# Kernel optimization log

Hardware: AMD Instinct MI355X
Metric: run time of the kernel (lower is better)

Reference implementation:

```python
import jax, jax.numpy as jnp
import numpy as np

B_GRAPHS = 16
N_PER_GRAPH = 128
N_NODES = B_GRAPHS * N_PER_GRAPH  # 2048
HIDDEN = 256
N_HEADS = 8
HEAD_DIM = HIDDEN // N_HEADS
N_LAYERS = 4
K_RPE = 4
N_EDGES = 32768
NUM_NODE_FEATS = 32
NUM_EDGE_TYPES = 16
MAX_DEGREE = 100
MLP_HID = HIDDEN // 2


def _layernorm(x, s, b):
    m = x.mean(-1, keepdims=True)
    v = jnp.var(x, axis=-1, keepdims=True)
    return (x - m) / jnp.sqrt(v + 1e-5) * s + b


def setup_inputs() -> dict:
    key = jax.random.key(0)
    ks = jax.random.split(key, 24)
    s = 0.02
    x_idx = jax.random.randint(ks[0], (N_NODES,), 0, NUM_NODE_FEATS)
    # edges are intra-graph (the torch code drops cross-graph edges)
    src = jax.random.randint(ks[1], (N_EDGES,), 0, N_NODES)
    dst = (src // N_PER_GRAPH) * N_PER_GRAPH + jax.random.randint(ks[2], (N_EDGES,), 0, N_PER_GRAPH)
    edge_index = jnp.stack([src, dst])
    edge_attr = jax.random.randint(ks[3], (N_EDGES,), 0, NUM_EDGE_TYPES)
    batch = jnp.repeat(jnp.arange(B_GRAPHS), N_PER_GRAPH)
    L = N_LAYERS
    return {
        'x_idx': x_idx, 'edge_index': edge_index, 'edge_attr': edge_attr, 'batch': batch,
        'node_emb': jax.random.normal(ks[4], (NUM_NODE_FEATS, HIDDEN)) * s,
        'edge_emb': jax.random.normal(ks[5], (NUM_EDGE_TYPES, N_HEADS)) * s,
        'degree_emb': jax.random.normal(ks[6], (MAX_DEGREE + 1, HIDDEN)) * s,
        'rpe_W1': jax.random.normal(ks[7], (K_RPE + 1, MLP_HID)) * s,
        'rpe_b1': jnp.zeros((MLP_HID,)),
        'rpe_W2': jax.random.normal(ks[8], (MLP_HID, N_HEADS)) * s,
        'rpe_b2': jnp.zeros((N_HEADS,)),
        'Wq': jax.random.normal(ks[9], (L, HIDDEN, HIDDEN)) * s, 'bq': jnp.zeros((L, HIDDEN)),
        'Wk': jax.random.normal(ks[10], (L, HIDDEN, HIDDEN)) * s, 'bk': jnp.zeros((L, HIDDEN)),
        'Wv': jax.random.normal(ks[11], (L, HIDDEN, HIDDEN)) * s, 'bv': jnp.zeros((L, HIDDEN)),
        'Wo': jax.random.normal(ks[12], (L, HIDDEN, HIDDEN)) * s, 'bo': jnp.zeros((L, HIDDEN)),
        'ln1_s': jnp.ones((L, HIDDEN)), 'ln1_b': jnp.zeros((L, HIDDEN)),
        'ln2_s': jnp.ones((L, HIDDEN)), 'ln2_b': jnp.zeros((L, HIDDEN)),
        'ff_W1': jax.random.normal(ks[13], (L, HIDDEN, 2 * HIDDEN)) * s, 'ff_b1': jnp.zeros((L, 2 * HIDDEN)),
        'ff_W2': jax.random.normal(ks[14], (L, 2 * HIDDEN, HIDDEN)) * s, 'ff_b2': jnp.zeros((L, HIDDEN)),
    }


def _forward(x_idx, edge_index, edge_attr, batch,
             node_emb, edge_emb, degree_emb, rpe_W1, rpe_b1, rpe_W2, rpe_b2,
             Wq, bq, Wk, bk, Wv, bv, Wo, bo, ln1_s, ln1_b, ln2_s, ln2_b,
             ff_W1, ff_b1, ff_W2, ff_b2):
    B, n, H, N = B_GRAPHS, N_PER_GRAPH, N_HEADS, N_NODES
    x = node_emb[x_idx]                               # [N, d]
    src, dst = edge_index[0], edge_index[1]
    # degrees from source endpoints (scatter_add in torch)
    deg = jnp.zeros((N,), jnp.int32).at[src].add(1)
    deg_c = jnp.minimum(deg, MAX_DEGREE)

    # ---- RRWP + edge-type attention bias, block-diagonal over graphs ----
    g = batch[src]
    intra = (batch[src] == batch[dst])                # torch code skips cross-graph edges
    u = src % n
    v = dst % n
    intra_f = intra.astype(jnp.float32)
    inv_du = intra_f / jnp.maximum(deg[src], 1).astype(jnp.float32)
    inv_dv = intra_f / jnp.maximum(deg[dst], 1).astype(jnp.float32)
    # random-walk transition matrix per graph [B, n, n]
    T = (jnp.zeros((B, n, n), jnp.float32)
         .at[g, u, v].add(inv_du)
         .at[g, v, u].add(inv_dv))
    # symmetric edge-type bias per graph [B, n, n, H]
    ev = edge_emb[edge_attr] * intra_f[:, None]
    EB = (jnp.zeros((B, n, n, H), jnp.float32)
          .at[g, u, v].add(ev)
          .at[g, v, u].add(ev))
    # walk powers I, T, T^2, ..., T^K -> [B, n, n, K+1]
    I = jnp.broadcast_to(jnp.eye(n, dtype=jnp.float32), (B, n, n))
    powers = [I, T]
    cur = T
    for _ in range(2, K_RPE + 1):
        cur = cur @ T
        powers.append(cur)
    walk = jnp.stack(powers, axis=-1)
    pair = jax.nn.relu(walk @ rpe_W1 + rpe_b1) @ rpe_W2 + rpe_b2   # [B, n, n, H]
    block = (pair + EB).transpose(0, 3, 1, 2)                      # [B, H, n, n]
    ib = jnp.arange(B)
    full = jnp.full((H, B, n, B, n), -jnp.inf, jnp.float32)
    full = full.at[:, ib, :, ib, :].set(block)                     # diag blocks
    attn_bias = full.reshape(H, N, N)

    # ---- transformer stack ----
    deg_vec = degree_emb[deg_c]
    scale = 1.0 / jnp.sqrt(jnp.float32(HEAD_DIM))
    for l in range(N_LAYERS):
        x = x + deg_vec
        Q = (x @ Wq[l] + bq[l]).reshape(N, H, HEAD_DIM)
        K_ = (x @ Wk[l] + bk[l]).reshape(N, H, HEAD_DIM)
        V = (x @ Wv[l] + bv[l]).reshape(N, H, HEAD_DIM)
        scores = jnp.einsum('ihd,jhd->hij', Q, K_) * scale + attn_bias
        aw = jax.nn.softmax(scores, axis=-1)
        out = jnp.einsum('hij,jhd->ihd', aw, V).reshape(N, HIDDEN)
        out = out @ Wo[l] + bo[l]
        x = _layernorm(x + out, ln1_s[l], ln1_b[l])
        ff = jax.nn.relu(x @ ff_W1[l] + ff_b1[l]) @ ff_W2[l] + ff_b2[l]
        x = _layernorm(x + ff, ln2_s[l], ln2_b[l])
    # global add pool
    return jax.ops.segment_sum(x, batch, num_segments=B)


def reference(x_idx, edge_index, edge_attr, batch,
              node_emb, edge_emb, degree_emb, rpe_W1, rpe_b1, rpe_W2, rpe_b2,
              Wq, bq, Wk, bk, Wv, bv, Wo, bo, ln1_s, ln1_b, ln2_s, ln2_b,
              ff_W1, ff_b1, ff_W2, ff_b2):
    return _forward(x_idx, edge_index, edge_attr, batch,
                    node_emb, edge_emb, degree_emb, rpe_W1, rpe_b1, rpe_W2, rpe_b2,
                    Wq, bq, Wk, bk, Wv, bv, Wo, bo, ln1_s, ln1_b, ln2_s, ln2_b,
                    ff_W1, ff_b1, ff_W2, ff_b2)
```

## Files before the change

kernel.cpp:

```cpp
#include <hip/hip_runtime.h>
#include <hip/hip_bf16.h>

#define B_GRAPHS 16
#define NPG 128
#define NN 2048
#define HIDDEN 256
#define N_HEADS 8
#define HEAD_DIM 32
#define N_LAYERS 4
#define N_EDGES 32768
#define MLP_HID 128
#define MAX_DEG 100

typedef __hip_bfloat16 bf16;
typedef unsigned short ushort_t;
typedef __attribute__((ext_vector_type(8))) short short8;
typedef __attribute__((ext_vector_type(4))) float f32x4;

__device__ __forceinline__ float us2f(ushort_t u) {
    return __uint_as_float(((unsigned)u) << 16);
}
__device__ __forceinline__ ushort_t f2us(float f) {
    unsigned u = __float_as_uint(f);
    return (ushort_t)((u + 0x7FFFu + ((u >> 16) & 1u)) >> 16);
}
__device__ __forceinline__ bool is_bf16_mode(const unsigned* probe) {
    return probe[0] != 0x3F800000u;
}
#define MFMA16(a, b, c) __builtin_amdgcn_mfma_f32_16x16x32_bf16(a, b, c, 0, 0, 0)

__device__ __forceinline__ void gload_lds16(const void* g, void* l) {
    __builtin_amdgcn_global_load_lds(
        (const __attribute__((address_space(1))) unsigned int*)g,
        (__attribute__((address_space(3))) unsigned int*)l, 16, 0, 0);
}
#define SBAR __builtin_amdgcn_s_barrier()
#define WAITP8 asm volatile("s_waitcnt vmcnt(8) lgkmcnt(0)" ::: "memory")
#define WAITLAST asm volatile("s_waitcnt vmcnt(0) lgkmcnt(0)" ::: "memory")
#define LBAR do { asm volatile("s_waitcnt lgkmcnt(0)" ::: "memory"); SBAR; \
                  asm volatile("" ::: "memory"); } while (0)

#define NW 23
__device__ const int c_wsizes[NW] = {
    8192, 128, 25856, 640, 128, 1024, 8,
    262144, 1024, 262144, 1024, 262144, 1024, 262144, 1024,
    1024, 1024, 1024, 1024,
    524288, 2048, 524288, 1024};
#define TOTW 2144392

#define OFF_NODE_EMB 0
#define OFF_EDGE_EMB 8192
#define OFF_DEG_EMB  8320
#define OFF_RPE_W1   34176
#define OFF_RPE_B1   34816
#define OFF_RPE_W2   34944
#define OFF_RPE_B2   35968
#define OFF_BO       1087624
#define OFF_LN1S     1088648
#define OFF_LN1B     1089672
#define OFF_LN2S     1090696
#define OFF_LN2B     1091720
#define OFF_FFB1     1617032
#define OFF_FFB2     2143368

#define WB_QKV 0
#define WB_O   786432
#define WB_F1  1048576
#define WB_F2  1572864
#define WB_TOT 2097152
#define QKVB_TOT 3072

#define ZERO_BLKS 2310
#define CONV_BLKS 8389
#define TP_BLKS   2048

struct SrcPtrs { const void* p[NW]; };

__global__ __launch_bounds__(256) void prep1(SrcPtrs sp, const unsigned* __restrict__ probe,
                                             float* __restrict__ Wc, float* __restrict__ qkvb,
                                             f32x4* __restrict__ zerop,
                                             ushort_t* __restrict__ WB) {
    __shared__ float tile[32][33];
    int b = blockIdx.x;
    bool isbf = is_bf16_mode(probe);
    auto rd = [&](int seg, int off) -> float {
        return isbf ? us2f(((const ushort_t*)sp.p[seg])[off])
                    : ((const float*)sp.p[seg])[off];
    };
    if (b < ZERO_BLKS) {
        f32x4 z;
        z[0] = 0.f; z[1] = 0.f; z[2] = 0.f; z[3] = 0.f;
        zerop[b * 256 + threadIdx.x] = z;
    } else if (b < ZERO_BLKS + CONV_BLKS) {
        int i = (b - ZERO_BLKS) * 256 + threadIdx.x;
        if (i < TOTW) {
            int seg = 0, off = i;
            while (seg < NW - 1 && off >= c_wsizes[seg]) { off -= c_wsizes[seg]; seg++; }
            bool dead = (seg == 7 || seg == 9 || seg == 11 || seg == 13 ||
                         seg == 19 || seg == 21);
            if (!dead) Wc[i] = rd(seg, off);
        } else if (i < TOTW + QKVB_TOT) {
            int j = i - TOTW;
            int l = j / 768, n = j % 768, which = n >> 8, nn = n & 255;
            int seg = (which == 0) ? 8 : (which == 1) ? 10 : 12;
            qkvb[j] = rd(seg, l * 256 + nn);
        }
    } else {
        int tb = b - ZERO_BLKS - CONV_BLKS;
        int seg, soff, srcN, k0, n0, dK;
        size_t doff;
        if (tb < 768) {
            int mat = tb >> 6, t = tb & 63;
            int l = mat / 3, which = mat % 3;
            seg = 7 + which * 2;
            soff = l * 65536; srcN = 256;
            k0 = (t >> 3) * 32; n0 = (t & 7) * 32;
            doff = (size_t)l * 196608 + (size_t)which * 65536; dK = 256;
        } else if (tb < 1024) {
            int u = tb - 768, l = u >> 6, t = u & 63;
            seg = 13; soff = l * 65536; srcN = 256;
            k0 = (t >> 3) * 32; n0 = (t & 7) * 32;
            doff = WB_O + (size_t)l * 65536; dK = 256;
        } else if (tb < 1536) {
            int u = tb - 1024, l = u >> 7, t = u & 127;
            seg = 19; soff = l * 131072; srcN = 512;
            k0 = (t >> 4) * 32; n0 = (t & 15) * 32;
            doff = WB_F1 + (size_t)l * 131072; dK = 256;
        } else {
            int u = tb - 1536, l = u >> 7, t = u & 127;
            seg = 21; soff = l * 131072; srcN = 256;
            k0 = (t >> 3) * 32; n0 = (t & 7) * 32;
            doff = WB_F2 + (size_t)l * 131072; dK = 512;
        }
        int xcol = threadIdx.x & 31, y8 = threadIdx.x >> 5;
        const void* srcp = sp.p[seg];
#pragma unroll
        for (int rr = 0; rr < 4; rr++) {
            int row = y8 * 4 + rr;
            int off = soff + (k0 + row) * srcN + n0 + xcol;
            tile[row][xcol] = isbf ? us2f(((const ushort_t*)srcp)[off])
                                   : ((const float*)srcp)[off];
        }
        __syncthreads();
#pragma unroll
        for (int rr = 0; rr < 4; rr++) {
            int nrow = y8 * 4 + rr;
            WB[doff + (size_t)(n0 + nrow) * dK + k0 + xcol] = f2us(tile[xcol][nrow]);
        }
    }
}

__global__ void deg_kernel(const int* __restrict__ src, int* __restrict__ deg) {
    int e = blockIdx.x * blockDim.x + threadIdx.x;
    if (e < N_EDGES) atomicAdd(&deg[src[e]], 1);
}

__global__ void prep2(const int* __restrict__ xidx, const int* __restrict__ deg,
                      const float* __restrict__ emb, const float* __restrict__ demb,
                      float* __restrict__ x, ushort_t* __restrict__ xb,
                      const int* __restrict__ ei, const int* __restrict__ eattr,
                      const int* __restrict__ batch, const float* __restrict__ edge_emb,
                      float* __restrict__ T, float* __restrict__ bias) {
    int b = blockIdx.x;
    if (b < 2048) {
        int i = b * 256 + threadIdx.x;
        int node = i >> 8, c = i & 255;
        float v = emb[xidx[node] * HIDDEN + c] + demb[min(deg[node], MAX_DEG) * HIDDEN + c];
        x[i] = v;
        xb[i] = f2us(v);
    } else {
        int idx = (b - 2048) * 256 + threadIdx.x;
        int e = idx >> 3, h = idx & 7;
        int s = ei[e], d = ei[N_EDGES + e];
        if (batch[s] != batch[d]) return;
        int g = batch[s];
        int u = s & (NPG - 1), v = d & (NPG - 1);
        if (h == 0) {
            atomicAdd(&T[(g * NPG + u) * NPG + v], 1.0f / (float)max(deg[s], 1));
            atomicAdd(&T[(g * NPG + v) * NPG + u], 1.0f / (float)max(deg[d], 1));
        }
        float ev = edge_emb[eattr[e] * N_HEADS + h];
        atomicAdd(&bias[(((size_t)(g * N_HEADS + h) * NPG + u) * NPG + v)], ev);
        atomicAdd(&bias[(((size_t)(g * N_HEADS + h) * NPG + v) * NPG + u)], ev);
    }
}

__global__ __launch_bounds__(256) void matmul128(const float* __restrict__ A,
                                                 const float* __restrict__ B,
                                                 float* __restrict__ C) {
    int g = blockIdx.x >> 4, t8 = blockIdx.x & 15;
    int col = threadIdx.x & 127, half = threadIdx.x >> 7;
    const float* Ag = A + (size_t)g * NPG * NPG;
    const float* Bg = B + (size_t)g * NPG * NPG;
    __shared__ float arow[8][NPG];
    for (int i = threadIdx.x; i < 8 * NPG; i += 256)
        arow[i >> 7][i & 127] = Ag[(t8 * 8 + (i >> 7)) * NPG + (i & 127)];
    __syncthreads();
    float acc[4] = {0.f, 0.f, 0.f, 0.f};
#pragma unroll 8
    for (int k = 0; k < NPG; k++) {
        float bv = Bg[k * NPG + col];
#pragma unroll
        for (int r = 0; r < 4; r++) acc[r] += arow[half * 4 + r][k] * bv;
    }
#pragma unroll
    for (int r = 0; r < 4; r++)
        C[((size_t)g * NPG + t8 * 8 + half * 4 + r) * NPG + col] = acc[r];
}

__global__ __launch_bounds__(256) void matmul128_dual(const float* __restrict__ T2,
                                                      const float* __restrict__ T,
                                                      float* __restrict__ T3,
                                                      float* __restrict__ T4) {
    int which = blockIdx.x >> 8;
    int bid = blockIdx.x & 255;
    int g = bid >> 4, t8 = bid & 15;
    int col = threadIdx.x & 127, half = threadIdx.x >> 7;
    const float* Ag = T2 + (size_t)g * NPG * NPG;
    const float* Bg = (which ? T2 : T) + (size_t)g * NPG * NPG;
    float* Cg = (which ? T4 : T3) + (size_t)g * NPG * NPG;
    __shared__ float arow[8][NPG];
    for (int i = threadIdx.x; i < 8 * NPG; i += 256)
        arow[i >> 7][i & 127] = Ag[(t8 * 8 + (i >> 7)) * NPG + (i & 127)];
    __syncthreads();
    float acc[4] = {0.f, 0.f, 0.f, 0.f};
#pragma unroll 8
    for (int k = 0; k < NPG; k++) {
        float bv = Bg[k * NPG + col];
#pragma unroll
        for (int r = 0; r < 4; r++) acc[r] += arow[half * 4 + r][k] * bv;
    }
#pragma unroll
    for (int r = 0; r < 4; r++)
        Cg[(t8 * 8 + half * 4 + r) * NPG + col] = acc[r];
}

__global__ __launch_bounds__(256) void rpe_kernel(
    const float* __restrict__ T, const float* __restrict__ T2,
    const float* __restrict__ T3, const float* __restrict__ T4,
    const float* __restrict__ W1, const float* __restrict__ b1,
    const float* __restrict__ W2, const float* __restrict__ b2,
    float* __restrict__ bias) {
    int g = blockIdx.x >> 7, i = blockIdx.x & 127;
    int w = threadIdx.x >> 6, lane = threadIdx.x & 63;
    int lr = lane & 15, lq = lane >> 4;
    __shared__ __align__(16) ushort_t hid[4][4096];

    int pbase = (g * 128 + i) * 128;
    int j0w = w * 32;

    f32x4 zero;
    zero[0] = 0.f; zero[1] = 0.f; zero[2] = 0.f; zero[3] = 0.f;

    short8 b1f[8];
#pragma unroll
    for (int nt = 0; nt < 8; nt++) {
        short8 v{};
        if (lq == 0) {
            int n = nt * 16 + lr;
#pragma unroll
            for (int e = 0; e < 5; e++) v[e] = (short)f2us(W1[e * 128 + n]);
        }
        b1f[nt] = v;
    }
    short8 b2f[4];
#pragma unroll
    for (int kt = 0; kt < 4; kt++) {
        short8 v{};
        if (lr < 8) {
#pragma unroll
            for (int e = 0; e < 8; e++)
                v[e] = (short)f2us(W2[(kt * 32 + lq * 8 + e) * 8 + lr]);
        }
        b2f[kt] = v;
    }
    float b1v[8];
#pragma unroll
    for (int nt = 0; nt < 8; nt++) b1v[nt] = b1[nt * 16 + lr];
    float b2v = (lr < 8) ? b2[lr] : 0.f;

#pragma unroll
    for (int mt = 0; mt < 2; mt++) {
        int j0 = j0w + mt * 16;
        short8 af{};
        if (lq == 0) {
            int p = pbase + j0 + lr;
            af[0] = (short)f2us((i == j0 + lr) ? 1.f : 0.f);
            af[1] = (short)f2us(T[p]);
            af[2] = (short)f2us(T2[p]);
            af[3] = (short)f2us(T3[p]);
            af[4] = (short)f2us(T4[p]);
        }
        f32x4 h[8];
#pragma unroll
        for (int nt = 0; nt < 8; nt++) h[nt] = MFMA16(af, b1f[nt], zero);
#pragma unroll
        for (int nt = 0; nt < 8; nt++) {
#pragma unroll
            for (int r = 0; r < 4; r++) {
                int row = mt * 16 + lq * 4 + r;
                int colb = (nt * 32 + lr * 2) ^ ((row & 7) << 4);
                *(ushort_t*)((char*)&hid[w][0] + row * 256 + colb) =
                    f2us(fmaxf(h[nt][r] + b1v[nt], 0.f));
            }
        }
    }
    asm volatile("s_waitcnt lgkmcnt(0)" ::: "memory");

#pragma unroll
    for (int mt = 0; mt < 2; mt++) {
        f32x4 o;
        o[0] = 0.f; o[1] = 0.f; o[2] = 0.f; o[3] = 0.f;
#pragma unroll
        for (int kt = 0; kt < 4; kt++) {
            int row = mt * 16 + lr;
            int colb = (kt * 64 + lq * 16) ^ ((lr & 7) << 4);
            short8 a = *(const short8*)((const char*)&hid[w][0] + row * 256 + colb);
            o = MFMA16(a, b2f[kt], o);
        }
        if (lr < 8) {
            size_t base2 = (((size_t)(g * N_HEADS + lr) * NPG + i) * NPG) + j0w + mt * 16;
#pragma unroll
            for (int r = 0; r < 4; r++)
                bias[base2 + lq * 4 + r] += o[r] + b2v;
        }
    }
}

__global__ __launch_bounds__(512, 1) void qkv_attn(
    const ushort_t* __restrict__ x_bf, const ushort_t* __restrict__ WT,
    const float* __restrict__ qb, const float* __restrict__ bias,
    ushort_t* __restrict__ ao) {
    int g = blockIdx.x >> 3, h = blockIdx.x & 7;
    int o = threadIdx.x >> 6, lane = threadIdx.x & 63;
    int lr = lane & 15, lq = lane >> 4;

    __shared__ char Wbuf[3][16384];
    __shared__ ushort_t Ks[NPG][40];
    __shared__ ushort_t VT[32][136];
    __shared__ ushort_t P[8][16][136];

    const ushort_t* xg = x_bf + (size_t)g * NPG * HIDDEN;
    int row16 = o * 16;

    short8 Ax[8];
#pragma unroll
    for (int kk = 0; kk < 8; kk++)
        Ax[kk] = *(const short8*)(xg + (size_t)(row16 + lr) * 256 + kk * 32 + lq * 8);
    float bqv[2], bkv[2], bvv[2];
#pragma unroll
    for (int j = 0; j < 2; j++) {
        int c = h * 32 + j * 16 + lr;
        bqv[j] = qb[c]; bkv[j] = qb[256 + c]; bvv[j] = qb[512 + c];
    }
    __builtin_amdgcn_sched_barrier(0);

    auto stageW = [&](int rowbase, int c) {
        const char* gW = (const char*)WT;
        char* lb = &Wbuf[c][0] + o * 2048;
#pragma unroll
        for (int it = 0; it < 2; it++) {
            int j = o * 2048 + it * 1024 + lane * 16;
            int n = j >> 9, off = j & 511;
            gload_lds16(gW + (size_t)(rowbase + n) * 512 + (off ^ ((n & 7) << 4)),
                        lb + it * 1024);
        }
        __builtin_amdgcn_sched_barrier(0);
    };
    stageW(h * 32, 0);
    stageW(256 + h * 32, 1);
    stageW(512 + h * 32, 2);

    auto rdW = [&](int c, int jt, int kk) -> short8 {
        int n = jt * 16 + lr;
        int off = n * 512 + ((kk * 64 + lq * 16) ^ ((n & 7) << 4));
        return *(const short8*)(&Wbuf[c][off]);
    };

    f32x4 qa[2]{}, ka[2]{}, va[2]{};
    asm volatile("s_waitcnt vmcnt(4)" ::: "memory"); SBAR;
#pragma unroll
    for (int kk = 0; kk < 8; kk++)
#pragma unroll
        for (int j = 0; j < 2; j++)
            qa[j] = MFMA16(Ax[kk], rdW(0, j, kk), qa[j]);

    const float* bg = bias + (size_t)(g * N_HEADS + h) * NPG * NPG;
    float bgv[8][4];
#pragma unroll
    for (int r = 0; r < 4; r++) {
        int i = row16 + lq * 4 + r;
#pragma unroll
        for (int jt = 0; jt < 8; jt++)
            bgv[jt][r] = bg[(size_t)i * NPG + jt * 16 + lr];
    }
    __builtin_amdgcn_sched_barrier(0);

    asm volatile("s_waitcnt vmcnt(34)" ::: "memory"); SBAR;
#pragma unroll
    for (int kk = 0; kk < 8; kk++)
#pragma unroll
        for (int j = 0; j < 2; j++)
            ka[j] = MFMA16(Ax[kk], rdW(1, j, kk), ka[j]);

    asm volatile("s_waitcnt vmcnt(32)" ::: "memory"); SBAR;
#pragma unroll
    for (int kk = 0; kk < 8; kk++)
#pragma unroll
        for (int j = 0; j < 2; j++)
            va[j] = MFMA16(Ax[kk], rdW(2, j, kk), va[j]);

#pragma unroll
    for (int j = 0; j < 2; j++) {
        int c = j * 16 + lr;
#pragma unroll
        for (int r = 0; r < 4; r++) {
            int row = row16 + lq * 4 + r;
            P[o][lq * 4 + r][c] = f2us(qa[j][r] + bqv[j]);
            Ks[row][c] = f2us(ka[j][r] + bkv[j]);
            VT[c][row] = f2us(va[j][r] + bvv[j]);
        }
    }
    __syncthreads();

    short8 qf = *(const short8*)(&P[o][lr][lq * 8]);
    f32x4 S[8];
    f32x4 zero;
    zero[0] = 0.f; zero[1] = 0.f; zero[2] = 0.f; zero[3] = 0.f;
#pragma unroll
    for (int jt = 0; jt < 8; jt++) {
        short8 kf = *(const short8*)(&Ks[jt * 16 + lr][lq * 8]);
        S[jt] = MFMA16(qf, kf, zero);
    }

    const float scale = 0.17677669529663687f;
    float lrow[4];
#pragma unroll
    for (int r = 0; r < 4; r++) {
        float mx = -1e30f;
#pragma unroll
        for (int jt = 0; jt < 8; jt++) {
            float s = S[jt][r] * scale + bgv[jt][r];
            S[jt][r] = s;
            mx = fmaxf(mx, s);
        }
#pragma unroll
        for (int m = 1; m < 16; m <<= 1) mx = fmaxf(mx, __shfl_xor(mx, m));
        float sum = 0.f;
#pragma unroll
        for (int jt = 0; jt < 8; jt++) {
            float e = __expf(S[jt][r] - mx);
            S[jt][r] = e;
            sum += e;
        }
#pragma unroll
        for (int m = 1; m < 16; m <<= 1) sum += __shfl_xor(sum, m);
        lrow[r] = sum;
    }

#pragma unroll
    for (int jt = 0; jt < 8; jt++)
#pragma unroll
        for (int r = 0; r < 4; r++)
            P[o][lq * 4 + r][jt * 16 + lr] = f2us(S[jt][r]);

    f32x4 O[2]{};
#pragma unroll
    for (int k0 = 0; k0 < NPG; k0 += 32) {
        short8 pa = *(const short8*)(&P[o][lr][k0 + lq * 8]);
#pragma unroll
        for (int dt = 0; dt < 2; dt++) {
            short8 vb = *(const short8*)(&VT[dt * 16 + lr][k0 + lq * 8]);
            O[dt] = MFMA16(pa, vb, O[dt]);
        }
    }
#pragma unroll
    for (int r = 0; r < 4; r++) {
        float inv = 1.f / lrow[r];
        int row = g * NPG + row16 + lq * 4 + r;
#pragma unroll
        for (int dt = 0; dt < 2; dt++)
            ao[(size_t)row * HIDDEN + h * 32 + dt * 16 + lr] = f2us(O[dt][r] * inv);
    }
}

__global__ __launch_bounds__(512, 2) void fused_mlp(
    const ushort_t* __restrict__ ao, const ushort_t* __restrict__ WoT,
    const float* __restrict__ bo, const float* __restrict__ ln1s,
    const float* __restrict__ ln1b,
    const ushort_t* __restrict__ F1T, const ushort_t* __restrict__ F2T,
    const float* __restrict__ fb1, const float* __restrict__ fb2,
    const float* __restrict__ ln2s, const float* __restrict__ ln2b,
    const float* __restrict__ xin, const int* __restrict__ deg,
    const float* __restrict__ demb, int add_deg,
    float* __restrict__ xout, ushort_t* __restrict__ xb,
    float* __restrict__ poolf, int do_pool) {
    int m0 = blockIdx.x * 8;
    int wave = threadIdx.x >> 6, lane = threadIdx.x & 63;
    int lr = lane & 15, lq = lane >> 4;
    int ar = m0 + (lr & 7);

    __shared__ ushort_t Wbuf[2][32768];
    __shared__ ushort_t xs_bf[8][264];
    __shared__ ushort_t ffh[8][520];
    __shared__ float ws[8][16], qs[8][16];

    auto stageO = [&](int h, int b) {
        const char* gW = (const char*)WoT;
        char* lb = (char*)&Wbuf[b][0] + wave * 8192;
#pragma unroll
        for (int it = 0; it < 8; it++) {
            int j = wave * 8192 + it * 1024 + lane * 16;
            int n = j >> 8, off = j & 255;
            gload_lds16(gW + n * 512 + h * 256 + (off ^ ((n & 7) << 4)), lb + it * 1024);
        }
        __builtin_amdgcn_sched_barrier(0);
    };
    auto stageF1 = [&](int q, int b) {
        const char* gW = (const char*)F1T;
        char* lb = (char*)&Wbuf[b][0] + wave * 8192;
#pragma unroll
        for (int it = 0; it < 8; it++) {
            int j = wave * 8192 + it * 1024 + lane * 16;
            int n = j >> 9, off = j & 511;
            gload_lds16(gW + (q * 128 + n) * 512 + (off ^ ((n & 7) << 4)), lb + it * 1024);
        }
        __builtin_amdgcn_sched_barrier(0);
    };
    auto stageF2 = [&](int q, int b) {
        const char* gW = (const char*)F2T;
        char* lb = (char*)&Wbuf[b][0] + wave * 8192;
#pragma unroll
        for (int it = 0; it < 8; it++) {
            int j = wave * 8192 + it * 1024 + lane * 16;
            int n = j >> 8, off = j & 255;
            gload_lds16(gW + n * 1024 + q * 256 + (off ^ ((n & 7) << 4)), lb + it * 1024);
        }
        __builtin_amdgcn_sched_barrier(0);
    };

    float bo_v[2], l1s[2], l1b[2], fb2v[2], l2s[2], l2b[2], xres[2][4], fb1q[4];
#pragma unroll
    for (int jt = 0; jt < 2; jt++) {
        int col = wave * 32 + jt * 16 + lr;
        bo_v[jt] = bo[col]; l1s[jt] = ln1s[col]; l1b[jt] = ln1b[col];
        fb2v[jt] = fb2[col]; l2s[jt] = ln2s[col]; l2b[jt] = ln2b[col];
#pragma unroll
        for (int r = 0; r < 4; r++) {
            int row = m0 + ((lq * 4 + r) & 7);
            xres[jt][r] = xin[(size_t)row * 256 + col];
        }
    }
#pragma unroll
    for (int q = 0; q < 4; q++) fb1q[q] = fb1[q * 128 + wave * 16 + lr];
    int dg4[4];
    if (add_deg) {
#pragma unroll
        for (int r = 0; r < 4; r++)
            dg4[r] = min(deg[m0 + ((lq * 4 + r) & 7)], MAX_DEG);
    }
    short8 Af[8];
#pragma unroll
    for (int t = 0; t < 8; t++)
        Af[t] = *(const short8*)(ao + (size_t)ar * 256 + t * 32 + lq * 8);

    stageO(0, 0);
    stageO(1, 1);

    f32x4 acc[2]{};
#pragma unroll
    for (int h = 0; h < 2; h++) {
        WAITP8; SBAR; asm volatile("" ::: "memory");
#pragma unroll
        for (int kk = 0; kk < 4; kk++) {
            short8 a = Af[h * 4 + kk];
#pragma unroll
            for (int jt = 0; jt < 2; jt++) {
                int n = wave * 32 + jt * 16 + lr;
                int bo_ = n * 256 + ((kk * 64 + lq * 16) ^ ((n & 7) << 4));
                short8 bf = *(const short8*)((const char*)&Wbuf[h][0] + bo_);
                acc[jt] = MFMA16(a, bf, acc[jt]);
            }
        }
        LBAR;
        if (h == 0) stageF1(0, 0);
        else        stageF1(1, 1);
    }

    float valLN[2][4];
#pragma unroll
    for (int r = 0; r < 4; r++) {
        float s = 0.f, s2 = 0.f;
#pragma unroll
        for (int jt = 0; jt < 2; jt++) {
            float v = acc[jt][r] + bo_v[jt] + xres[jt][r];
            valLN[jt][r] = v;
            s += v;
            s2 += v * v;
        }
#pragma unroll
        for (int m = 1; m < 16; m <<= 1) {
            s += __shfl_xor(s, m);
            s2 += __shfl_xor(s2, m);
        }
        if (lr == 0) { ws[wave][lq * 4 + r] = s; qs[wave][lq * 4 + r] = s2; }
    }
    LBAR;
#pragma unroll
    for (int r = 0; r < 4; r++) {
        int rr = lq * 4 + r;
        float sum = 0.f, sum2 = 0.f;
#pragma unroll
        for (int c = 0; c < 8; c++) { sum += ws[c][rr]; sum2 += qs[c][rr]; }
        float mean = sum * (1.f / 256.f);
        float var = sum2 * (1.f / 256.f) - mean * mean;
        float rstd = rsqrtf(var + 1e-5f);
#pragma unroll
        for (int jt = 0; jt < 2; jt++) {
            int col = wave * 32 + jt * 16 + lr;
            float y = (valLN[jt][r] - mean) * rstd * l1s[jt] + l1b[jt];
            valLN[jt][r] = y;
            if (rr < 8) xs_bf[rr][col] = f2us(y);
        }
    }

#pragma unroll
    for (int q = 0; q < 4; q++) {
        WAITP8; SBAR; asm volatile("" ::: "memory");
        f32x4 a1{};
        int nl = wave * 16 + lr;
#pragma unroll
        for (int kk = 0; kk < 8; kk++) {
            short8 a = *(const short8*)(&xs_bf[lr & 7][kk * 32 + lq * 8]);
            int bo_ = nl * 512 + ((kk * 64 + lq * 16) ^ ((nl & 7) << 4));
            short8 bf = *(const short8*)((const char*)&Wbuf[q & 1][0] + bo_);
            a1 = MFMA16(a, bf, a1);
        }
        int col = q * 128 + wave * 16 + lr;
#pragma unroll
        for (int r = 0; r < 4; r++) {
            int rr = lq * 4 + r;
            if (rr < 8) ffh[rr][col] = f2us(fmaxf(a1[r] + fb1q[q], 0.f));
        }
        LBAR;
        if (q < 2) stageF1(q + 2, q & 1);
        else       stageF2(q - 2, q & 1);
    }

    f32x4 acc2[2]{};
#pragma unroll
    for (int q = 0; q < 4; q++) {
        if (q == 3) { WAITLAST; } else { WAITP8; }
        SBAR; asm volatile("" ::: "memory");
#pragma unroll
        for (int kk = 0; kk < 4; kk++) {
            short8 a = *(const short8*)(&ffh[lr & 7][q * 128 + kk * 32 + lq * 8]);
#pragma unroll
            for (int jt = 0; jt < 2; jt++) {
                int n = wave * 32 + jt * 16 + lr;
                int bo_ = n * 256 + ((kk * 64 + lq * 16) ^ ((n & 7) << 4));
                short8 bf = *(const short8*)((const char*)&Wbuf[q & 1][0] + bo_);
                acc2[jt] = MFMA16(a, bf, acc2[jt]);
            }
        }
        LBAR;
        if (q < 2) stageF2(q + 2, q & 1);
    }

    float val2[2][4];
#pragma unroll
    for (int r = 0; r < 4; r++) {
        int rr = lq * 4 + r;
        float s = 0.f, s2 = 0.f;
#pragma unroll
        for (int jt = 0; jt < 2; jt++) {
            float v = acc2[jt][r] + fb2v[jt] + valLN[jt][r];
            val2[jt][r] = v;
            s += v;
            s2 += v * v;
        }
#pragma unroll
        for (int m = 1; m < 16; m <<= 1) {
            s += __shfl_xor(s, m);
            s2 += __shfl_xor(s2, m);
        }
        if (lr == 0) { ws[wave][rr] = s; qs[wave][rr] = s2; }
    }
    __syncthreads();
    float psum[2] = {0.f, 0.f};
#pragma unroll
    for (int r = 0; r < 4; r++) {
        int rr = lq * 4 + r;
        float sum = 0.f, sum2 = 0.f;
#pragma unroll
        for (int c = 0; c < 8; c++) { sum += ws[c][rr]; sum2 += qs[c][rr]; }
        float mean = sum * (1.f / 256.f);
        float var = sum2 * (1.f / 256.f) - mean * mean;
        float rstd = rsqrtf(var + 1e-5f);
        if (rr < 8) {
            int row = m0 + rr;
#pragma unroll
            for (int jt = 0; jt < 2; jt++) {
                int col = wave * 32 + jt * 16 + lr;
                float y = (val2[jt][r] - mean) * rstd * l2s[jt] + l2b[jt];
                if (add_deg) y += demb[dg4[r] * 256 + col];
                xout[(size_t)row * 256 + col] = y;
                xb[(size_t)row * 256 + col] = f2us(y);
                if (do_pool) psum[jt] += y;
            }
        }
    }
    if (do_pool && lq < 2) {
        int g = m0 >> 7;
#pragma unroll
        for (int jt = 0; jt < 2; jt++) {
            int col = wave * 32 + jt * 16 + lr;
            atomicAdd(&poolf[g * 256 + col], psum[jt]);
        }
    }
}

__global__ void pool_kernel(const float* __restrict__ poolf, void* __restrict__ out,
                            const unsigned* __restrict__ probe) {
    int i = blockIdx.x * 256 + threadIdx.x;
    float acc = poolf[i];
    if (is_bf16_mode(probe))
        ((bf16*)out)[i] = __float2bfloat16(acc);
    else
        ((float*)out)[i] = acc;
}

extern "C" void kernel_launch(void* const* d_in, const int* in_sizes, int n_in,
                              void* d_out, int out_size, void* d_ws, size_t ws_size,
                              hipStream_t stream) {
    const int* x_idx      = (const int*)d_in[0];
    const int* edge_index = (const int*)d_in[1];
    const int* edge_attr  = (const int*)d_in[2];
    const int* batch      = (const int*)d_in[3];
    const unsigned* probe = (const unsigned*)d_in[19];

    char* base = (char*)d_ws;
    float* Wc    = (float*)base;       base += (size_t)TOTW * 4;
    float* x     = (float*)base;       base += (size_t)NN * HIDDEN * 4;
    float* T     = (float*)base;       base += 262144 * 4;
    float* bias  = (float*)base;       base += (size_t)2097152 * 4;
    int*   deg   = (int*)base;         base += 2048 * 4;
    float* poolf = (float*)base;       base += 4096 * 4;
    float* T2    = (float*)base;       base += 262144 * 4;
    float* T3    = (float*)base;       base += 262144 * 4;
    float* T4    = (float*)base;       base += 262144 * 4;
    float* qkvb  = (float*)base;       base += QKVB_TOT * 4;
    ushort_t* WB    = (ushort_t*)base; base += (size_t)WB_TOT * 2;
    ushort_t* x_bf  = (ushort_t*)base; base += (size_t)NN * HIDDEN * 2;
    ushort_t* ao_bf = (ushort_t*)base; base += (size_t)NN * HIDDEN * 2;

    SrcPtrs sp;
    for (int i = 0; i < NW; i++) sp.p[i] = d_in[4 + i];

    prep1<<<ZERO_BLKS + CONV_BLKS + TP_BLKS, 256, 0, stream>>>(sp, probe, Wc, qkvb,
                                                               (f32x4*)T, WB);
    deg_kernel<<<N_EDGES / 256, 256, 0, stream>>>(edge_index, deg);
    prep2<<<3072, 256, 0, stream>>>(x_idx, deg, Wc + OFF_NODE_EMB, Wc + OFF_DEG_EMB,
                                    x, x_bf, edge_index, edge_attr, batch,
                                    Wc + OFF_EDGE_EMB, T, bias);
    matmul128<<<256, 256, 0, stream>>>(T, T, T2);
    matmul128_dual<<<512, 256, 0, stream>>>(T2, T, T3, T4);
    rpe_kernel<<<B_GRAPHS * NPG, 256, 0, stream>>>(
        T, T2, T3, T4, Wc + OFF_RPE_W1, Wc + OFF_RPE_B1, Wc + OFF_RPE_W2, Wc + OFF_RPE_B2,
        bias);

    for (int l = 0; l < N_LAYERS; l++) {
        qkv_attn<<<B_GRAPHS * N_HEADS, 512, 0, stream>>>(
            x_bf, WB + WB_QKV + (size_t)l * 196608, qkvb + l * 768, bias, ao_bf);
        fused_mlp<<<NN / 8, 512, 0, stream>>>(
            ao_bf, WB + WB_O + (size_t)l * 65536, Wc + OFF_BO + l * 256,
            Wc + OFF_LN1S + l * 256, Wc + OFF_LN1B + l * 256,
            WB + WB_F1 + (size_t)l * 131072, WB + WB_F2 + (size_t)l * 131072,
            Wc + OFF_FFB1 + l * 512, Wc + OFF_FFB2 + l * 256,
            Wc + OFF_LN2S + l * 256, Wc + OFF_LN2B + l * 256, x,
            deg, Wc + OFF_DEG_EMB, (l < N_LAYERS - 1) ? 1 : 0, x, x_bf,
            poolf, (l == N_LAYERS - 1) ? 1 : 0);
    }
    pool_kernel<<<16, 256, 0, stream>>>(poolf, d_out, probe);
}
```

Measured before the change: 308.2 us.

## Fuse T3/T4 matmuls into RPE MLP kernel via shared-memory rows

Merges the dual 128x128 matmul kernel that computed T3=T2@T and T4=T2@T2 into the RPE MLP kernel. Each block computes 8 rows of T3/T4 into shared memory and runs the MFMA MLP on them directly, so the T3/T4 global buffers and one launch go away. The grid shrinks from 2048 blocks to 256, and each wave now handles 8x more (i,j) pairs serially, which may reduce parallelism and latency hiding.

```diff
diff --git a/kernel.cpp b/kernel.cpp
--- a/kernel.cpp
+++ b/kernel.cpp
@@ -208,46 +208,22 @@
         C[((size_t)g * NPG + t8 * 8 + half * 4 + r) * NPG + col] = acc[r];
 }
 
-__global__ __launch_bounds__(256) void matmul128_dual(const float* __restrict__ T2,
-                                                      const float* __restrict__ T,
-                                                      float* __restrict__ T3,
-                                                      float* __restrict__ T4) {
-    int which = blockIdx.x >> 8;
-    int bid = blockIdx.x & 255;
-    int g = bid >> 4, t8 = bid & 15;
-    int col = threadIdx.x & 127, half = threadIdx.x >> 7;
-    const float* Ag = T2 + (size_t)g * NPG * NPG;
-    const float* Bg = (which ? T2 : T) + (size_t)g * NPG * NPG;
-    float* Cg = (which ? T4 : T3) + (size_t)g * NPG * NPG;
-    __shared__ float arow[8][NPG];
-    for (int i = threadIdx.x; i < 8 * NPG; i += 256)
-        arow[i >> 7][i & 127] = Ag[(t8 * 8 + (i >> 7)) * NPG + (i & 127)];
-    __syncthreads();
-    float acc[4] = {0.f, 0.f, 0.f, 0.f};
-#pragma unroll 8
-    for (int k = 0; k < NPG; k++) {
-        float bv = Bg[k * NPG + col];
-#pragma unroll
-        for (int r = 0; r < 4; r++) acc[r] += arow[half * 4 + r][k] * bv;
-    }
-#pragma unroll
-    for (int r = 0; r < 4; r++)
-        Cg[(t8 * 8 + half * 4 + r) * NPG + col] = acc[r];
-}
-
-__global__ __launch_bounds__(256) void rpe_kernel(
-    const float* __restrict__ T, const float* __restrict__ T2,
-    const float* __restrict__ T3, const float* __restrict__ T4,
+__global__ __launch_bounds__(256) void dual_rpe(
+    const float* __restrict__ T, const float* __restrict__ T2c,
     const float* __restrict__ W1, const float* __restrict__ b1,
     const float* __restrict__ W2, const float* __restrict__ b2,
     float* __restrict__ bias) {
-    int g = blockIdx.x >> 7, i = blockIdx.x & 127;
-    int w = threadIdx.x >> 6, lane = threadIdx.x & 63;
+    int g = blockIdx.x >> 4, t8 = blockIdx.x & 15;
+    int tid = threadIdx.x;
+    int w = tid >> 6, lane = tid & 63;
     int lr = lane & 15, lq = lane >> 4;
+
+    __shared__ float arow[8][NPG];
+    __shared__ float T3L[8][NPG], T4L[8][NPG];
     __shared__ __align__(16) ushort_t hid[4][4096];
 
-    int pbase = (g * 128 + i) * 128;
-    int j0w = w * 32;
+    const float* Tg  = T   + (size_t)g * NPG * NPG;
+    const float* T2g = T2c + (size_t)g * NPG * NPG;
 
     f32x4 zero;
     zero[0] = 0.f; zero[1] = 0.f; zero[2] = 0.f; zero[3] = 0.f;
@@ -279,50 +255,83 @@
     for (int nt = 0; nt < 8; nt++) b1v[nt] = b1[nt * 16 + lr];
     float b2v = (lr < 8) ? b2[lr] : 0.f;
 
-#pragma unroll
-    for (int mt = 0; mt < 2; mt++) {
-        int j0 = j0w + mt * 16;
-        short8 af{};
-        if (lq == 0) {
-            int p = pbase + j0 + lr;
-            af[0] = (short)f2us((i == j0 + lr) ? 1.f : 0.f);
-            af[1] = (short)f2us(T[p]);
-            af[2] = (short)f2us(T2[p]);
-            af[3] = (short)f2us(T3[p]);
-            af[4] = (short)f2us(T4[p]);
-        }
-        f32x4 h[8];
-#pragma unroll
-        for (int nt = 0; nt < 8; nt++) h[nt] = MFMA16(af, b1f[nt], zero);
-#pragma unroll
-        for (int nt = 0; nt < 8; nt++) {
+    int col = tid & 127, half = tid >> 7;
+    for (int i = tid; i < 8 * NPG; i += 256)
+        arow[i >> 7][i & 127] = T2g[(t8 * 8 + (i >> 7)) * NPG + (i & 127)];
+    __syncthreads();
+    {
+        float a3[4] = {0.f, 0.f, 0.f, 0.f}, a4[4] = {0.f, 0.f, 0.f, 0.f};
+#pragma unroll 8
+        for (int k = 0; k < NPG; k++) {
+            float bv3 = Tg[k * NPG + col];
+            float bv4 = T2g[k * NPG + col];
 #pragma unroll
             for (int r = 0; r < 4; r++) {
-                int row = mt * 16 + lq * 4 + r;
-                int colb = (nt * 32 + lr * 2) ^ ((row & 7) << 4);
-                *(ushort_t*)((char*)&hid[w][0] + row * 256 + colb) =
-                    f2us(fmaxf(h[nt][r] + b1v[nt], 0.f));
+                float av = arow[half * 4 + r][k];
+                a3[r] += av * bv3;
+                a4[r] += av * bv4;
             }
         }
-    }
-    asm volatile("s_waitcnt lgkmcnt(0)" ::: "memory");
-
-#pragma unroll
-    for (int mt = 0; mt < 2; mt++) {
-        f32x4 o;
-        o[0] = 0.f; o[1] = 0.f; o[2] = 0.f; o[3] = 0.f;
-#pragma unroll
-        for (int kt = 0; kt < 4; kt++) {
-            int row = mt * 16 + lr;
-            int colb = (kt * 64 + lq * 16) ^ ((lr & 7) << 4);
-            short8 a = *(const short8*)((const char*)&hid[w][0] + row * 256 + colb);
-            o = MFMA16(a, b2f[kt], o);
-        }
-        if (lr < 8) {
-            size_t base2 = (((size_t)(g * N_HEADS + lr) * NPG + i) * NPG) + j0w + mt * 16;
-#pragma unroll
-            for (int r = 0; r < 4; r++)
-                bias[base2 + lq * 4 + r] += o[r] + b2v;
+#pragma unroll
+        for (int r = 0; r < 4; r++) {
+            T3L[half * 4 + r][col] = a3[r];
+            T4L[half * 4 + r][col] = a4[r];
+        }
+    }
+    __syncthreads();
+
+#pragma unroll
+    for (int il = 0; il < 2; il++) {
+        int iloc = w * 2 + il;
+        int gi = t8 * 8 + iloc;
+#pragma unroll
+        for (int jp = 0; jp < 4; jp++) {
+#pragma unroll
+            for (int mt = 0; mt < 2; mt++) {
+                int j0 = jp * 32 + mt * 16;
+                short8 af{};
+                if (lq == 0) {
+                    int j = j0 + lr;
+                    af[0] = (short)f2us((gi == j) ? 1.f : 0.f);
+                    af[1] = (short)f2us(Tg[gi * NPG + j]);
+                    af[2] = (short)f2us(T2g[gi * NPG + j]);
+                    af[3] = (short)f2us(T3L[iloc][j]);
+                    af[4] = (short)f2us(T4L[iloc][j]);
+                }
+                f32x4 h[8];
+#pragma unroll
+                for (int nt = 0; nt < 8; nt++) h[nt] = MFMA16(af, b1f[nt], zero);
+#pragma unroll
+                for (int nt = 0; nt < 8; nt++) {
+#pragma unroll
+                    for (int r = 0; r < 4; r++) {
+                        int row = mt * 16 + lq * 4 + r;
+                        int colb = (nt * 32 + lr * 2) ^ ((row & 7) << 4);
+                        *(ushort_t*)((char*)&hid[w][0] + row * 256 + colb) =
+                            f2us(fmaxf(h[nt][r] + b1v[nt], 0.f));
+                    }
+                }
+            }
+            asm volatile("s_waitcnt lgkmcnt(0)" ::: "memory");
+#pragma unroll
+            for (int mt = 0; mt < 2; mt++) {
+                f32x4 o;
+                o[0] = 0.f; o[1] = 0.f; o[2] = 0.f; o[3] = 0.f;
+#pragma unroll
+                for (int kt = 0; kt < 4; kt++) {
+                    int row = mt * 16 + lr;
+                    int colb = (kt * 64 + lq * 16) ^ ((lr & 7) << 4);
+                    short8 a = *(const short8*)((const char*)&hid[w][0] + row * 256 + colb);
+                    o = MFMA16(a, b2f[kt], o);
+                }
+                if (lr < 8) {
+                    size_t base2 = (((size_t)(g * N_HEADS + lr) * NPG + gi) * NPG) +
+                                   jp * 32 + mt * 16;
+#pragma unroll
+                    for (int r = 0; r < 4; r++)
+                        bias[base2 + lq * 4 + r] += o[r] + b2v;
+                }
+            }
         }
     }
 }
@@ -747,8 +756,6 @@
     int*   deg   = (int*)base;         base += 2048 * 4;
     float* poolf = (float*)base;       base += 4096 * 4;
     float* T2    = (float*)base;       base += 262144 * 4;
-    float* T3    = (float*)base;       base += 262144 * 4;
-    float* T4    = (float*)base;       base += 262144 * 4;
     float* qkvb  = (float*)base;       base += QKVB_TOT * 4;
     ushort_t* WB    = (ushort_t*)base; base += (size_t)WB_TOT * 2;
     ushort_t* x_bf  = (ushort_t*)base; base += (size_t)NN * HIDDEN * 2;
@@ -764,9 +771,8 @@
                                     x, x_bf, edge_index, edge_attr, batch,
                                     Wc + OFF_EDGE_EMB, T, bias);
     matmul128<<<256, 256, 0, stream>>>(T, T, T2);
-    matmul128_dual<<<512, 256, 0, stream>>>(T2, T, T3, T4);
-    rpe_kernel<<<B_GRAPHS * NPG, 256, 0, stream>>>(
-        T, T2, T3, T4, Wc + OFF_RPE_W1, Wc + OFF_RPE_B1, Wc + OFF_RPE_W2, Wc + OFF_RPE_B2,
+    dual_rpe<<<256, 256, 0, stream>>>(
+        T, T2, Wc + OFF_RPE_W1, Wc + OFF_RPE_B1, Wc + OFF_RPE_W2, Wc + OFF_RPE_B2,
         bias);
 
     for (int l = 0; l < N_LAYERS; l++) {
```

Result: no change. 311.9 us (+1.2%).
